# Performance work log

Measured on AMD Instinct MI355X. Metric: run time of the kernel, lower is better.

Reference implementation:

```python
import jax, jax.numpy as jnp
import numpy as np

EPS = 1e-5

def _conv3x3(x, w, b):
    # NCHW, OIHW, 3x3 stride 1 pad 1
    y = jax.lax.conv_general_dilated(x, w, window_strides=(1, 1),
                                     padding=((1, 1), (1, 1)),
                                     dimension_numbers=('NCHW', 'OIHW', 'NCHW'))
    return y + b[None, :, None, None]

def _pool_upsample(x, k):
    # adaptive avg pool to (H/k, W/k) then nearest block-upsample back
    B, C, H, W = x.shape
    p = x.reshape(B, C, H // k, k, W // k, k).mean(axis=(3, 5))
    return jnp.repeat(jnp.repeat(p, k, axis=2), k, axis=3)

def setup_inputs() -> dict:
    key = jax.random.key(0)
    ks = jax.random.split(key, 12)
    B, C, H, W = 32, 8, 300, 300
    d = {
        'x': jax.random.normal(ks[0], (B, C, H, W), jnp.float32),
        'w5': jax.random.normal(ks[1], (8, 16, 3, 3), jnp.float32) * 0.1,
        'b5': jnp.zeros((8,), jnp.float32),
        'w10': jax.random.normal(ks[2], (8, 16, 3, 3), jnp.float32) * 0.1,
        'b10': jnp.zeros((8,), jnp.float32),
        'w15': jax.random.normal(ks[3], (8, 16, 3, 3), jnp.float32) * 0.1,
        'b15': jnp.zeros((8,), jnp.float32),
        'gw': jax.random.normal(ks[4], (8, 24, 3, 3), jnp.float32) * 0.1,
        'gb': jnp.zeros((8,), jnp.float32),
        'mw': jax.random.normal(ks[5], (8, 24, 3, 3), jnp.float32) * 0.1,
        'mb': jnp.zeros((8,), jnp.float32),
        'gamma': jnp.ones((8,), jnp.float32),
        'beta': jnp.zeros((8,), jnp.float32),
    }
    return d

def reference(x, w5, b5, w10, b10, w15, b15, gw, gb, mw, mb, gamma, beta):
    up5 = _pool_upsample(x, 5)    # [B,8,300,300]
    up10 = _pool_upsample(x, 10)
    up15 = _pool_upsample(x, 15)
    c5 = _conv3x3(jnp.concatenate([x, up5], axis=1), w5, b5)
    c10 = _conv3x3(jnp.concatenate([x, up10], axis=1), w10, b10)
    c15 = _conv3x3(jnp.concatenate([x, up15], axis=1), w15, b15)
    g_in = jnp.concatenate([c5, c10, c15], axis=1)  # [B,24,H,W]
    # gated conv, activation=None: conv(g_in) * sigmoid(mask_conv(g_in))
    y = _conv3x3(g_in, gw, gb) * jax.nn.sigmoid(_conv3x3(g_in, mw, mb))
    # batch norm (training-mode batch stats, biased var, as torch default)
    mean = y.mean(axis=(0, 2, 3), keepdims=True)
    var = ((y - mean) ** 2).mean(axis=(0, 2, 3), keepdims=True)
    y = (y - mean) * jax.lax.rsqrt(var + EPS)
    return y * gamma[None, :, None, None] + beta[None, :, None, None]
```

## Files before the change

### kernel.cpp

```cpp
#include <hip/hip_runtime.h>
#include <math.h>

typedef __bf16 bfrag __attribute__((ext_vector_type(8)));
typedef __bf16 bf16x4 __attribute__((ext_vector_type(4)));
typedef __bf16 bf16x8 __attribute__((ext_vector_type(8)));
typedef float f32x4 __attribute__((ext_vector_type(4)));

#define BN 32
#define HH 300
#define WW 300
#define HW 90000
#define NPX (BN * HW)

#define GX 10
#define GY 19
#define CPX 612
#define XPX 720
#define CWSTRIDE 4896

#define P5I_BYTE_OFF   0
#define P10I_BYTE_OFF  1843200
#define P15I_BYTE_OFF  2304000
#define CWB_BYTE_OFF   2508800
#define GWB_BYTE_OFF   2524160
#define STAT_BYTE_OFF  2531328
#define SS_BYTE_OFF    2539520
#define XBF_BYTE_OFF   2539584
#define XBF_END        (XBF_BYTE_OFF + (size_t)NPX * 16)
#define GW3_BYTE_OFF   XBF_END
#define NEW3_END       (GW3_BYTE_OFF + 9216)

#define XU3_OFF   0
#define P5_OFF3   11520
#define P10_OFF3  12160
#define P15_OFF3  12400
#define CW0_OFF3  12592
#define CW1_OFF3  22384
#define LDS3_SIZE 32176

__device__ __forceinline__ short f2bf(float f) {
    union { float f; unsigned u; } v;
    v.f = f;
    unsigned r = v.u + 0x7FFF + ((v.u >> 16) & 1);
    return (short)(r >> 16);
}

__device__ __forceinline__ float bf2f(unsigned short s) {
    union { unsigned u; float f; } v;
    v.u = ((unsigned)s) << 16;
    return v.f;
}

__device__ __forceinline__ void setup_body(int gid, int gstride,
                                           const float* __restrict__ w5,
                                           const float* __restrict__ w10,
                                           const float* __restrict__ w15,
                                           const float* __restrict__ gw,
                                           const float* __restrict__ mw,
                                           short* __restrict__ cBg,
                                           short* __restrict__ gBg,
                                           short* __restrict__ gB3,
                                           double* __restrict__ stats) {
    for (int idx = gid; idx < 7680; idx += gstride) {
        int s = idx / 2560, rem = idx % 2560;
        int n = rem / 160, r2 = rem % 160;
        int tap = r2 / 16, ci = r2 % 16;
        float v = 0.f;
        if (n < 8 && tap < 9) {
            const float* W = (s == 0) ? w5 : ((s == 1) ? w10 : w15);
            v = W[(n * 16 + ci) * 9 + tap];
        }
        cBg[idx] = f2bf(v);
    }
    for (int idx = gid; idx < 3584; idx += gstride) {
        int n = idx / 224, r2 = idx % 224;
        int blk = r2 / 8, cj = r2 % 8;
        float v = 0.f;
        if (blk < 27) {
            int tap = blk / 3, ci24 = (blk % 3) * 8 + cj;
            if (n < 8) v = gw[(n * 24 + ci24) * 9 + tap];
            else       v = mw[((n - 8) * 24 + ci24) * 9 + tap];
        }
        gBg[idx] = f2bf(v);
    }
    if (gB3) {
        for (int idx = gid; idx < 4608; idx += gstride) {
            int s = idx / 1536, rem = idx % 1536;
            int n = rem / 96, r2 = rem % 96;
            int slot = r2 / 8, cj = r2 % 8;
            float v = 0.f;
            if (slot < 9) {
                int ci24 = s * 8 + cj;
                if (n < 8) v = gw[(n * 24 + ci24) * 9 + slot];
                else       v = mw[((n - 8) * 24 + ci24) * 9 + slot];
            }
            gB3[idx] = f2bf(v);
        }
    }
    for (int idx = gid; idx < 16 * 64; idx += gstride) stats[idx] = 0.0;
}

__global__ void k_setup(const float* __restrict__ w5, const float* __restrict__ w10,
                        const float* __restrict__ w15, const float* __restrict__ gw,
                        const float* __restrict__ mw, short* __restrict__ cBg,
                        short* __restrict__ gBg, double* __restrict__ stats) {
    setup_body(threadIdx.x, 256, w5, w10, w15, gw, mw, cBg, gBg, nullptr, stats);
}

__global__ __launch_bounds__(256) void k_xbf(const float* __restrict__ x,
                                             unsigned short* __restrict__ xbf,
                                             const float* __restrict__ w5,
                                             const float* __restrict__ w10,
                                             const float* __restrict__ w15,
                                             const float* __restrict__ gw,
                                             const float* __restrict__ mw,
                                             short* __restrict__ cBg,
                                             short* __restrict__ gBg,
                                             short* __restrict__ gB3,
                                             double* __restrict__ stats) {
    const int b = blockIdx.y;
    const int px = blockIdx.x * 256 + threadIdx.x;
    if (px < HW) {
        const float* xp = x + (size_t)b * 8 * HW + px;
        bf16x8 pk;
#pragma unroll
        for (int ch = 0; ch < 8; ch++) pk[ch] = (__bf16)xp[(size_t)ch * HW];
        *(bf16x8*)&xbf[((size_t)b * HW + px) * 8] = pk;
    }
    if (blockIdx.y == 0 && blockIdx.x < 16) {
        int gid = blockIdx.x * 256 + threadIdx.x;
        setup_body(gid, 4096, w5, w10, w15, gw, mw, cBg, gBg, gB3, stats);
    }
}

__global__ __launch_bounds__(256) void k_pool5b(const unsigned short* __restrict__ xbf,
                                                unsigned short* __restrict__ p5i) {
    int id = blockIdx.x * 256 + threadIdx.x;
    int b = id / 3600, cell = id % 3600;
    int pi = cell / 60, pj = cell % 60;
    const unsigned short* base = xbf + ((size_t)b * HW + pi * 5 * WW + pj * 5) * 8;
    float s[8] = {0.f, 0.f, 0.f, 0.f, 0.f, 0.f, 0.f, 0.f};
#pragma unroll
    for (int u = 0; u < 5; u++)
#pragma unroll
        for (int v = 0; v < 5; v++) {
            bf16x8 vv = *(const bf16x8*)&base[(u * WW + v) * 8];
#pragma unroll
            for (int ch = 0; ch < 8; ch++) s[ch] += (float)vv[ch];
        }
    bf16x8 pk;
#pragma unroll
    for (int ch = 0; ch < 8; ch++) pk[ch] = (__bf16)(s[ch] * 0.04f);
    *(bf16x8*)&p5i[((size_t)b * 3600 + cell) * 8] = pk;
}

__global__ void k_poolD(const unsigned short* __restrict__ p5i,
                        unsigned short* __restrict__ p10i,
                        unsigned short* __restrict__ p15i) {
    int id = blockIdx.x * 256 + threadIdx.x;
    if (id < 230400) {
        int bc = id / 900, cell = id % 900;
        int b = bc >> 3, c = bc & 7;
        int pi = cell / 30, pj = cell % 30;
        const unsigned short* base = p5i + ((size_t)b * 3600) * 8 + c;
        float s = bf2f(base[((2 * pi) * 60 + 2 * pj) * 8]) +
                  bf2f(base[((2 * pi) * 60 + 2 * pj + 1) * 8]) +
                  bf2f(base[((2 * pi + 1) * 60 + 2 * pj) * 8]) +
                  bf2f(base[((2 * pi + 1) * 60 + 2 * pj + 1) * 8]);
        p10i[((size_t)b * 900 + cell) * 8 + c] = (unsigned short)f2bf(s * 0.25f);
    } else if (id < 332800) {
        int id2 = id - 230400;
        int bc = id2 / 400, cell = id2 % 400;
        int b = bc >> 3, c = bc & 7;
        int pi = cell / 20, pj = cell % 20;
        const unsigned short* base = p5i + ((size_t)b * 3600) * 8 + c;
        float s = 0.f;
#pragma unroll
        for (int u = 0; u < 3; u++)
#pragma unroll
            for (int v = 0; v < 3; v++)
                s += bf2f(base[((3 * pi + u) * 60 + 3 * pj + v) * 8]);
        p15i[((size_t)b * 400 + cell) * 8 + c] = (unsigned short)f2bf(s * (1.f / 9.f));
    }
}

template <int K, int PCOLS>
__device__ __forceinline__ void c_phase3(char* LDSp, int cwOff, int patchOff,
                                         const unsigned short* __restrict__ cBs,
                                         const float* __restrict__ bias,
                                         int pr0, int pc0,
                                         int r0, int c0, int lane, int wid, bool edge) {
    constexpr int T0[5] = {0, 2, 4, 6, 8};
    constexpr int T1[5] = {1, 3, 5, 7, 8};
    const int n = lane & 15, quad = lane >> 4;
    const int qh = quad >> 1, ql = quad & 1;
    bfrag wfr[5];
#pragma unroll
    for (int km = 0; km < 5; km++) {
        int tapw = km * 2 + qh;
        wfr[km] = *(const bfrag*)&cBs[(n * 10 + tapw) * 16 + ql * 8];
    }
    const int srow = patchOff - pr0 * (PCOLS * 16);
    const int scol = -(pc0 << 4);
    float bO[4];
#pragma unroll
    for (int r = 0; r < 4; r++) bO[r] = bias[(quad & 1) * 4 + r];

    for (int g = wid; g < 39; g += 4) {
        int px = g * 16 + n;
        if (px > 611) px = 611;
        int rp = (int)((unsigned)px / 34u);
        int cp = px - rp * 34;
        int xb = (rp * 36 + cp) * 16;
        int rowB[3], colB[3];
#pragma unroll
        for (int d = 0; d < 3; d++) {
            rowB[d] = (int)(((unsigned)(r0 - 2 + rp + d + K) / (unsigned)K) * (PCOLS * 16)) + srow;
            colB[d] = (int)(((unsigned)(c0 - 2 + cp + d + K) / (unsigned)K) << 4) + scol;
        }
        f32x4 acc = {0.f, 0.f, 0.f, 0.f};
#pragma unroll
        for (int km = 0; km < 5; km++) {
            int au0 = rowB[T0[km] / 3] + colB[T0[km] % 3];
            int au1 = rowB[T1[km] / 3] + colB[T1[km] % 3];
            int ax0 = xb + ((T0[km] / 3) * 36 + (T0[km] % 3)) * 16;
            int ax1 = xb + ((T1[km] / 3) * 36 + (T1[km] % 3)) * 16;
            int au = qh ? au1 : au0;
            int ax = qh ? ax1 : ax0;
            int ad = ql ? au : ax;
            acc = __builtin_amdgcn_mfma_f32_16x16x32_bf16(
                wfr[km], *(const bfrag*)(LDSp + ad), acc, 0, 0, 0);
        }
        if (quad < 2) {
            bf16x4 pk;
#pragma unroll
            for (int r = 0; r < 4; r++) pk[r] = (__bf16)(acc[r] + bO[r]);
            if (edge) {
                int ra = r0 - 1 + rp, ca = c0 - 1 + cp;
                if (ra < 0 || ra >= HH || ca < 0 || ca >= WW) {
#pragma unroll
                    for (int r = 0; r < 4; r++) pk[r] = (__bf16)0.f;
                }
            }
            *(bf16x4*)(LDSp + cwOff + px * 16 + quad * 8) = pk;
        }
    }
}

__device__ __forceinline__ void gate_partial(const char* LDSp, int cwOff,
                                             const unsigned short* __restrict__ gB3s,
                                             int lane, int wid, f32x4* acc) {
    const int n = lane & 15, quad = lane >> 4;
    bfrag gfr[3];
    int goffB[3];
#pragma unroll
    for (int km = 0; km < 3; km++) {
        int slot = km * 4 + quad;
        int tap = (slot > 8) ? 8 : slot;
        gfr[km] = *(const bfrag*)&gB3s[(n * 12 + slot) * 8];
        int di = tap / 3, dj = tap - di * 3;
        goffB[km] = (di * 34 + dj) * 16;
    }
#pragma unroll
    for (int gi = 0; gi < 8; gi++) {
        int g = wid + 4 * gi;
        int px = g * 16 + n;
        int off0 = cwOff + ((px >> 5) * 34 + (px & 31)) * 16;
#pragma unroll
        for (int km = 0; km < 3; km++)
            acc[gi] = __builtin_amdgcn_mfma_f32_16x16x32_bf16(
                gfr[km], *(const bfrag*)(LDSp + off0 + goffB[km]), acc[gi], 0, 0, 0);
    }
}

__global__ __launch_bounds__(256, 5) void k_fused3(
    const unsigned short* __restrict__ xbf,
    const unsigned short* __restrict__ p5i, const unsigned short* __restrict__ p10i,
    const unsigned short* __restrict__ p15i,
    const unsigned short* __restrict__ cBg, const unsigned short* __restrict__ gB3,
    const float* __restrict__ b5, const float* __restrict__ b10, const float* __restrict__ b15,
    const float* __restrict__ gb, const float* __restrict__ mb,
    float* __restrict__ out, double* __restrict__ stats) {
    __shared__ __align__(16) char LDS[LDS3_SIZE];

    const int b = blockIdx.z;
    const int r0 = blockIdx.y * 16, c0 = blockIdx.x * 32;
    const int t = threadIdx.x, lane = t & 63, wid = t >> 6;
    const bool edge = (blockIdx.x == 0) | (blockIdx.x == GX - 1) |
                      (blockIdx.y == 0) | (blockIdx.y == GY - 1);

    const int pr0_5 = (r0 + 3) / 5, pc0_5 = (c0 + 3) / 5;
    const int pr0_10 = (r0 + 8) / 10, pc0_10 = (c0 + 8) / 10;
    const int pr0_15 = (r0 + 13) / 15, pc0_15 = (c0 + 13) / 15;

#pragma unroll
    for (int it = 0; it < 3; it++) {
        int idx = t + 256 * it;
        if (idx < XPX) {
            int i = idx / 36, j = idx - i * 36;
            int ra = r0 - 2 + i, ca = c0 - 2 + j;
            uint4 v = {0u, 0u, 0u, 0u};
            if (ra >= 0 && ra < HH && ca >= 0 && ca < WW)
                v = *(const uint4*)&xbf[((size_t)b * HW + ra * WW + ca) * 8];
            *(uint4*)(LDS + XU3_OFF + idx * 16) = v;
        }
    }
    if (t < 67) {
        const unsigned short* src;
        int off;
        bool valid;
        if (t < 40) {
            int a = t >> 3, cc = t & 7;
            int ci = pr0_5 - 1 + a, cj = pc0_5 - 1 + cc;
            valid = (ci >= 0) && (ci < 60) && (cj >= 0) && (cj < 60);
            src = p5i + ((size_t)b * 3600 + ci * 60 + cj) * 8;
            off = P5_OFF3 + t * 16;
        } else if (t < 55) {
            int i2 = t - 40;
            int a = i2 / 5, cc = i2 % 5;
            int ci = pr0_10 - 1 + a, cj = pc0_10 - 1 + cc;
            valid = (ci >= 0) && (ci < 30) && (cj >= 0) && (cj < 30);
            src = p10i + ((size_t)b * 900 + ci * 30 + cj) * 8;
            off = P10_OFF3 + i2 * 16;
        } else {
            int i2 = t - 55;
            int a = i2 >> 2, cc = i2 & 3;
            int ci = pr0_15 - 1 + a, cj = pc0_15 - 1 + cc;
            valid = (ci >= 0) && (ci < 20) && (cj >= 0) && (cj < 20);
            src = p15i + ((size_t)b * 400 + ci * 20 + cj) * 8;
            off = P15_OFF3 + i2 * 16;
        }
        uint4 v = {0u, 0u, 0u, 0u};
        if (valid) v = *(const uint4*)src;
        *(uint4*)(LDS + off) = v;
    }
    __syncthreads();

    f32x4 acc[8];
#pragma unroll
    for (int gi = 0; gi < 8; gi++) acc[gi] = (f32x4){0.f, 0.f, 0.f, 0.f};

    c_phase3<5, 8>(LDS, CW0_OFF3, P5_OFF3, cBg, b5, pr0_5, pc0_5, r0, c0, lane, wid, edge);
    __syncthreads();
    gate_partial(LDS, CW0_OFF3, gB3, lane, wid, acc);
    c_phase3<10, 5>(LDS, CW1_OFF3, P10_OFF3, cBg + 2560, b10, pr0_10, pc0_10, r0, c0, lane, wid, edge);
    __syncthreads();
    gate_partial(LDS, CW1_OFF3, gB3 + 1536, lane, wid, acc);
    c_phase3<15, 4>(LDS, CW0_OFF3, P15_OFF3, cBg + 5120, b15, pr0_15, pc0_15, r0, c0, lane, wid, edge);
    __syncthreads();
    gate_partial(LDS, CW0_OFF3, gB3 + 3072, lane, wid, acc);

    const int n = lane & 15, quad = lane >> 4;
    float gO[4], mO[4];
#pragma unroll
    for (int r = 0; r < 4; r++) {
        gO[r] = gb[(quad & 1) * 4 + r];
        mO[r] = mb[(quad & 1) * 4 + r];
    }
    float ls[4] = {0.f, 0.f, 0.f, 0.f}, ls2[4] = {0.f, 0.f, 0.f, 0.f};
#pragma unroll
    for (int gi = 0; gi < 8; gi++) {
        int g = wid + 4 * gi;
        int px = g * 16 + n;
        int rr = px >> 5, cc = px & 31;
        int ra = r0 + rr, ca = c0 + cc;
        bool wr = !edge || (ra < HH && ca < WW);
#pragma unroll
        for (int reg = 0; reg < 4; reg++) {
            float val;
            if (quad < 2) val = acc[gi][reg] + gO[reg];
            else          val = __builtin_amdgcn_rcpf(1.f + __expf(-(acc[gi][reg] + mO[reg])));
            float other = __shfl_xor(val, 32);
            if (quad < 2 && wr) {
                float y = val * other;
                int ch = quad * 4 + reg;
                out[(size_t)(b * 8 + ch) * HW + (size_t)ra * WW + ca] = y;
                ls[reg] += y;
                ls2[reg] += y * y;
            }
        }
    }
#pragma unroll
    for (int m = 1; m < 16; m <<= 1) {
#pragma unroll
        for (int r = 0; r < 4; r++) {
            ls[r] += __shfl_xor(ls[r], m);
            ls2[r] += __shfl_xor(ls2[r], m);
        }
    }
    if (n == 0 && quad < 2) {
        int hash = (blockIdx.x + GX * blockIdx.y + GX * GY * blockIdx.z) & 63;
#pragma unroll
        for (int r = 0; r < 4; r++) {
            atomicAdd(&stats[(quad * 4 + r) * 64 + hash], (double)ls[r]);
            atomicAdd(&stats[(8 + quad * 4 + r) * 64 + hash], (double)ls2[r]);
        }
    }
}

__global__ void k_pool5(const float* __restrict__ x, unsigned short* __restrict__ p5i) {
    int id = blockIdx.x * 256 + threadIdx.x;
    int bc = id / 3600, cell = id % 3600;
    int b = bc >> 3, c = bc & 7;
    int pi = cell / 60, pj = cell % 60;
    const float* rp = x + (size_t)bc * HW + pi * 5 * WW + pj * 5;
    float s = 0.f;
#pragma unroll
    for (int u = 0; u < 5; u++)
#pragma unroll
        for (int v = 0; v < 5; v++) s += rp[u * WW + v];
    p5i[((size_t)b * 3600 + cell) * 8 + c] = (unsigned short)f2bf(s * 0.04f);
}

template <int K, int PW>
__device__ __forceinline__ void up_load(const unsigned short* __restrict__ pooled,
                                        int b, int r0, int c0, int t, uint4* v) {
#pragma unroll
    for (int it = 0; it < 3; it++) {
        int idx = t + 256 * it;
        uint4 val = {0u, 0u, 0u, 0u};
        if (idx < XPX) {
            int i = idx / 36, j = idx - i * 36;
            int ra = r0 - 2 + i, ca = c0 - 2 + j;
            if (ra >= 0 && ra < HH && ca >= 0 && ca < WW) {
                int pi = (int)((unsigned)ra / K);
                int pj = (int)((unsigned)ca / K);
                val = *(const uint4*)&pooled[((size_t)b * (PW * PW) + pi * PW + pj) * 8];
            }
        }
        v[it] = val;
    }
}

__device__ __forceinline__ void up_store(short* xuU, int t, const uint4* v) {
#pragma unroll
    for (int it = 0; it < 3; it++) {
        int idx = t + 256 * it;
        if (idx < XPX) *(uint4*)&xuU[idx * 8] = v[it];
    }
}

__device__ __forceinline__ void c_phase(const short* xuX, const short* xuU,
                                        short* cwP,
                                        const unsigned short* __restrict__ cBs,
                                        const float* __restrict__ bias,
                                        int r0, int c0, int lane, int wid, bool edge) {
    const int n = lane & 15, quad = lane >> 4;
    const int qh = quad >> 1, ql = quad & 1;
    const short* xbase = ql ? xuU : xuX;
    bfrag wfr[5];
    int dpoff[5];
#pragma unroll
    for (int km = 0; km < 5; km++) {
        int tapw = km * 2 + qh;
        int tapa = (tapw > 8) ? 8 : tapw;
        wfr[km] = *(const bfrag*)&cBs[(n * 10 + tapw) * 16 + ql * 8];
        dpoff[km] = ((tapa / 3) * 36 + tapa % 3) * 8;
    }
    float bO[4];
#pragma unroll
    for (int r = 0; r < 4; r++) bO[r] = bias[(quad & 1) * 4 + r];

    for (int g = wid; g < 39; g += 4) {
        int px = g * 16 + n;
        if (px > 611) px = 611;
        int rp = (int)((unsigned)px / 34u);
        int cp = px - rp * 34;
        int pb = (rp * 36 + cp) * 8;
        f32x4 acc = {0.f, 0.f, 0.f, 0.f};
#pragma unroll
        for (int km = 0; km < 5; km++)
            acc = __builtin_amdgcn_mfma_f32_16x16x32_bf16(
                wfr[km], *(const bfrag*)&xbase[pb + dpoff[km]], acc, 0, 0, 0);
        if (quad < 2) {
            bf16x4 pk;
#pragma unroll
            for (int r = 0; r < 4; r++) pk[r] = (__bf16)(acc[r] + bO[r]);
            if (edge) {
                int ra = r0 - 1 + rp, ca = c0 - 1 + cp;
                if (ra < 0 || ra >= HH || ca < 0 || ca >= WW) {
#pragma unroll
                    for (int r = 0; r < 4; r++) pk[r] = (__bf16)0.f;
                }
            }
            *(bf16x4*)&cwP[px * 8 + quad * 4] = pk;
        }
    }
}

template <bool XBF>
__global__ __launch_bounds__(256, 3) void k_fused(
    const float* __restrict__ x, const unsigned short* __restrict__ xbf,
    const unsigned short* __restrict__ p5i, const unsigned short* __restrict__ p10i,
    const unsigned short* __restrict__ p15i,
    const unsigned short* __restrict__ cBg, const unsigned short* __restrict__ gBg,
    const float* __restrict__ b5, const float* __restrict__ b10, const float* __restrict__ b15,
    const float* __restrict__ gb, const float* __restrict__ mb,
    float* __restrict__ out, double* __restrict__ stats) {
    __shared__ __align__(16) short xuX[XPX * 8];
    __shared__ __align__(16) short xuU[XPX * 8];
    __shared__ __align__(16) short cwS[3 * CWSTRIDE];

    const int b = blockIdx.z;
    const int r0 = blockIdx.y * 16, c0 = blockIdx.x * 32;
    const int t = threadIdx.x, lane = t & 63, wid = t >> 6;
    const bool edge = (blockIdx.x == 0) | (blockIdx.x == GX - 1) |
                      (blockIdx.y == 0) | (blockIdx.y == GY - 1);

    uint4 upv[3];
    up_load<5, 60>(p5i, b, r0, c0, t, upv);

    if constexpr (XBF) {
#pragma unroll
        for (int it = 0; it < 3; it++) {
            int idx = t + 256 * it;
            if (idx < XPX) {
                int i = idx / 36, j = idx - i * 36;
                int ra = r0 - 2 + i, ca = c0 - 2 + j;
                uint4 v = {0u, 0u, 0u, 0u};
                if (ra >= 0 && ra < HH && ca >= 0 && ca < WW)
                    v = *(const uint4*)&xbf[((size_t)b * HW + ra * WW + ca) * 8];
                *(uint4*)&xuX[idx * 8] = v;
            }
        }
    } else {
        for (int idx = t; idx < 1440; idx += 256) {
            int cp = idx / 360, rem = idx % 360;
            int i = rem / 18, jp = rem % 18;
            int j = 2 * jp;
            int ra = r0 - 2 + i, ca = c0 - 2 + j;
            float2 v0 = {0.f, 0.f}, v1 = {0.f, 0.f};
            if (ra >= 0 && ra < HH && ca >= 0 && ca <= WW - 2) {
                size_t base = ((size_t)(b * 8 + 2 * cp) * HH + ra) * WW + ca;
                v0 = *(const float2*)&x[base];
                v1 = *(const float2*)&x[base + HW];
            }
            unsigned pA = (unsigned short)f2bf(v0.x) | ((unsigned)(unsigned short)f2bf(v1.x) << 16);
            unsigned pB = (unsigned short)f2bf(v0.y) | ((unsigned)(unsigned short)f2bf(v1.y) << 16);
            int px = i * 36 + j;
            *(unsigned*)&xuX[px * 8 + 2 * cp] = pA;
            *(unsigned*)&xuX[(px + 1) * 8 + 2 * cp] = pB;
        }
    }
    up_store(xuU, t, upv);
    __syncthreads();

    c_phase(xuX, xuU, cwS, cBg, b5, r0, c0, lane, wid, edge);
    up_load<10, 30>(p10i, b, r0, c0, t, upv);
    __syncthreads();
    up_store(xuU, t, upv);
    __syncthreads();

    c_phase(xuX, xuU, cwS + CWSTRIDE, cBg + 2560, b10, r0, c0, lane, wid, edge);
    up_load<15, 20>(p15i, b, r0, c0, t, upv);
    __syncthreads();
    up_store(xuU, t, upv);
    __syncthreads();

    c_phase(xuX, xuU, cwS + 2 * CWSTRIDE, cBg + 5120, b15, r0, c0, lane, wid, edge);
    __syncthreads();

    const int n = lane & 15, quad = lane >> 4;
    bfrag gfr[7];
    int goff[7];
#pragma unroll
    for (int km = 0; km < 7; km++) {
        int blkw = km * 4 + quad;
        int blka = (blkw > 26) ? 26 : blkw;
        gfr[km] = *(const bfrag*)&gBg[(n * 28 + blkw) * 8];
        int tap = blka / 3, cig = blka - tap * 3;
        goff[km] = cig * CWSTRIDE + ((tap / 3) * 34 + tap % 3) * 8;
    }
    float gO[4], mO[4];
#pragma unroll
    for (int r = 0; r < 4; r++) {
        gO[r] = gb[(quad & 1) * 4 + r];
        mO[r] = mb[(quad & 1) * 4 + r];
    }
    float ls[4] = {0.f, 0.f, 0.f, 0.f}, ls2[4] = {0.f, 0.f, 0.f, 0.f};

    for (int g = wid; g < 32; g += 4) {
        int px = g * 16 + n;
        int rr = px >> 5, cc = px & 31;
        int off0 = (rr * 34 + cc) * 8;
        f32x4 acc = {0.f, 0.f, 0.f, 0.f};
#pragma unroll
        for (int km = 0; km < 7; km++)
            acc = __builtin_amdgcn_mfma_f32_16x16x32_bf16(
                gfr[km], *(const bfrag*)&cwS[off0 + goff[km]], acc, 0, 0, 0);
        int ra = r0 + rr, ca = c0 + cc;
        bool wr = !edge || (ra < HH && ca < WW);
#pragma unroll
        for (int reg = 0; reg < 4; reg++) {
            float val;
            if (quad < 2) val = acc[reg] + gO[reg];
            else          val = __builtin_amdgcn_rcpf(1.f + __expf(-(acc[reg] + mO[reg])));
            float other = __shfl_xor(val, 32);
            if (quad < 2 && wr) {
                float y = val * other;
                int ch = quad * 4 + reg;
                out[(size_t)(b * 8 + ch) * HW + (size_t)ra * WW + ca] = y;
                ls[reg] += y;
                ls2[reg] += y * y;
            }
        }
    }
#pragma unroll
    for (int m = 1; m < 16; m <<= 1) {
#pragma unroll
        for (int r = 0; r < 4; r++) {
            ls[r] += __shfl_xor(ls[r], m);
            ls2[r] += __shfl_xor(ls2[r], m);
        }
    }
    if (n == 0 && quad < 2) {
        int hash = (blockIdx.x + GX * blockIdx.y + GX * GY * blockIdx.z) & 63;
#pragma unroll
        for (int r = 0; r < 4; r++) {
            atomicAdd(&stats[(quad * 4 + r) * 64 + hash], (double)ls[r]);
            atomicAdd(&stats[(8 + quad * 4 + r) * 64 + hash], (double)ls2[r]);
        }
    }
}

__global__ void k_stats(const double* __restrict__ stats, const float* __restrict__ gamma,
                        const float* __restrict__ beta, float* __restrict__ ss) {
    __shared__ double red[16][16];
    int t = threadIdx.x;
    int row = t >> 4, col = t & 15;
    double s = stats[row * 64 + col] + stats[row * 64 + col + 16] +
               stats[row * 64 + col + 32] + stats[row * 64 + col + 48];
    red[row][col] = s;
    __syncthreads();
    if (t < 16) {
        double tot = 0.0;
#pragma unroll
        for (int i = 0; i < 16; i++) tot += red[t][i];
        red[t][0] = tot;
    }
    __syncthreads();
    if (t < 8) {
        double N = (double)NPX;
        double mean = red[t][0] / N;
        double var = red[8 + t][0] / N - mean * mean;
        double scale = (double)gamma[t] / sqrt(var + 1e-5);
        ss[t] = (float)scale;
        ss[8 + t] = (float)((double)beta[t] - mean * scale);
    }
}

__global__ void k_norm(float* __restrict__ out, const float* __restrict__ ss) {
    int i = blockIdx.x * 256 + threadIdx.x;
    if (i < (BN * 8 * HW) / 4) {
        int plane = (i * 4) / HW;
        int ch = plane & 7;
        float sc = ss[ch], sh = ss[8 + ch];
        float4* p = (float4*)out + i;
        float4 v = *p;
        v.x = v.x * sc + sh;
        v.y = v.y * sc + sh;
        v.z = v.z * sc + sh;
        v.w = v.w * sc + sh;
        *p = v;
    }
}

extern "C" void kernel_launch(void* const* d_in, const int* in_sizes, int n_in,
                              void* d_out, int out_size, void* d_ws, size_t ws_size,
                              hipStream_t stream) {
    const float* x = (const float*)d_in[0];
    const float* w5 = (const float*)d_in[1];
    const float* b5 = (const float*)d_in[2];
    const float* w10 = (const float*)d_in[3];
    const float* b10 = (const float*)d_in[4];
    const float* w15 = (const float*)d_in[5];
    const float* b15 = (const float*)d_in[6];
    const float* gw = (const float*)d_in[7];
    const float* gb = (const float*)d_in[8];
    const float* mw = (const float*)d_in[9];
    const float* mb = (const float*)d_in[10];
    const float* gamma = (const float*)d_in[11];
    const float* beta = (const float*)d_in[12];
    float* out = (float*)d_out;

    unsigned short* p5i = (unsigned short*)((char*)d_ws + P5I_BYTE_OFF);
    unsigned short* p10i = (unsigned short*)((char*)d_ws + P10I_BYTE_OFF);
    unsigned short* p15i = (unsigned short*)((char*)d_ws + P15I_BYTE_OFF);
    short* cBg = (short*)((char*)d_ws + CWB_BYTE_OFF);
    short* gBg = (short*)((char*)d_ws + GWB_BYTE_OFF);
    double* stats = (double*)((char*)d_ws + STAT_BYTE_OFF);
    float* ss = (float*)((char*)d_ws + SS_BYTE_OFF);
    unsigned short* xbf = (unsigned short*)((char*)d_ws + XBF_BYTE_OFF);
    short* gB3 = (short*)((char*)d_ws + GW3_BYTE_OFF);

    dim3 grid(GX, GY, BN);
    if (ws_size >= NEW3_END) {
        k_xbf<<<dim3(352, 32), 256, 0, stream>>>(x, xbf, w5, w10, w15, gw, mw,
                                                 cBg, gBg, gB3, stats);
        k_pool5b<<<450, 256, 0, stream>>>(xbf, p5i);
        k_poolD<<<1300, 256, 0, stream>>>(p5i, p10i, p15i);
        k_fused3<<<grid, 256, 0, stream>>>(xbf, p5i, p10i, p15i,
                                           (const unsigned short*)cBg, (const unsigned short*)gB3,
                                           b5, b10, b15, gb, mb, out, stats);
    } else if (ws_size >= XBF_END) {
        k_xbf<<<dim3(352, 32), 256, 0, stream>>>(x, xbf, w5, w10, w15, gw, mw,
                                                 cBg, gBg, nullptr, stats);
        k_pool5b<<<450, 256, 0, stream>>>(xbf, p5i);
        k_poolD<<<1300, 256, 0, stream>>>(p5i, p10i, p15i);
        k_fused<true><<<grid, 256, 0, stream>>>(x, xbf, p5i, p10i, p15i,
                                                (const unsigned short*)cBg, (const unsigned short*)gBg,
                                                b5, b10, b15, gb, mb, out, stats);
    } else {
        k_setup<<<1, 256, 0, stream>>>(w5, w10, w15, gw, mw, cBg, gBg, stats);
        k_pool5<<<3600, 256, 0, stream>>>(x, p5i);
        k_poolD<<<1300, 256, 0, stream>>>(p5i, p10i, p15i);
        k_fused<false><<<grid, 256, 0, stream>>>(x, xbf, p5i, p10i, p15i,
                                                 (const unsigned short*)cBg, (const unsigned short*)gBg,
                                                 b5, b10, b15, gb, mb, out, stats);
    }
    k_stats<<<1, 256, 0, stream>>>(stats, gamma, beta, ss);
    k_norm<<<(BN * 8 * HW / 4 + 255) / 256, 256, 0, stream>>>(out, ss);
}
```

Before: 424.6 us.

## Fuse pooling levels into one kernel and keep all three branch outputs in LDS

Merges the 5x5 pooling and the derived 10x10/15x15 pooling into one tiled kernel that stages a 30x30 xbf tile in shared memory, removing one launch and the round trip of p5i. The fused conv kernel now computes all three branch convolutions into separate LDS buffers, then runs a single 7-step MFMA gated conv over 24 channels. This replaces the earlier interleaved per-branch gate partial accumulation. LDS use grows to about 42KB per block, which may reduce occupancy below the 3-block launch bound, and the extra setup path for gB3 is dropped.

```diff
diff --git a/kernel.cpp b/kernel.cpp
--- a/kernel.cpp
+++ b/kernel.cpp
@@ -27,16 +27,13 @@
 #define SS_BYTE_OFF    2539520
 #define XBF_BYTE_OFF   2539584
 #define XBF_END        (XBF_BYTE_OFF + (size_t)NPX * 16)
-#define GW3_BYTE_OFF   XBF_END
-#define NEW3_END       (GW3_BYTE_OFF + 9216)
-
-#define XU3_OFF   0
-#define P5_OFF3   11520
-#define P10_OFF3  12160
-#define P15_OFF3  12400
-#define CW0_OFF3  12592
-#define CW1_OFF3  22384
-#define LDS3_SIZE 32176
+
+#define XU4_OFF   0
+#define P5_OFF4   11520
+#define P10_OFF4  12160
+#define P15_OFF4  12400
+#define CW4_OFF   12592
+#define LDS4_SIZE 41968
 
 __device__ __forceinline__ short f2bf(float f) {
     union { float f; unsigned u; } v;
@@ -59,7 +56,6 @@
                                            const float* __restrict__ mw,
                                            short* __restrict__ cBg,
                                            short* __restrict__ gBg,
-                                           short* __restrict__ gB3,
                                            double* __restrict__ stats) {
     for (int idx = gid; idx < 7680; idx += gstride) {
         int s = idx / 2560, rem = idx % 2560;
@@ -83,20 +79,6 @@
         }
         gBg[idx] = f2bf(v);
     }
-    if (gB3) {
-        for (int idx = gid; idx < 4608; idx += gstride) {
-            int s = idx / 1536, rem = idx % 1536;
-            int n = rem / 96, r2 = rem % 96;
-            int slot = r2 / 8, cj = r2 % 8;
-            float v = 0.f;
-            if (slot < 9) {
-                int ci24 = s * 8 + cj;
-                if (n < 8) v = gw[(n * 24 + ci24) * 9 + slot];
-                else       v = mw[((n - 8) * 24 + ci24) * 9 + slot];
-            }
-            gB3[idx] = f2bf(v);
-        }
-    }
     for (int idx = gid; idx < 16 * 64; idx += gstride) stats[idx] = 0.0;
 }
 
@@ -104,7 +86,7 @@
                         const float* __restrict__ w15, const float* __restrict__ gw,
                         const float* __restrict__ mw, short* __restrict__ cBg,
                         short* __restrict__ gBg, double* __restrict__ stats) {
-    setup_body(threadIdx.x, 256, w5, w10, w15, gw, mw, cBg, gBg, nullptr, stats);
+    setup_body(threadIdx.x, 256, w5, w10, w15, gw, mw, cBg, gBg, stats);
 }
 
 __global__ __launch_bounds__(256) void k_xbf(const float* __restrict__ x,
@@ -116,7 +98,6 @@
                                              const float* __restrict__ mw,
                                              short* __restrict__ cBg,
                                              short* __restrict__ gBg,
-                                             short* __restrict__ gB3,
                                              double* __restrict__ stats) {
     const int b = blockIdx.y;
     const int px = blockIdx.x * 256 + threadIdx.x;
@@ -129,29 +110,279 @@
     }
     if (blockIdx.y == 0 && blockIdx.x < 16) {
         int gid = blockIdx.x * 256 + threadIdx.x;
-        setup_body(gid, 4096, w5, w10, w15, gw, mw, cBg, gBg, gB3, stats);
-    }
-}
-
-__global__ __launch_bounds__(256) void k_pool5b(const unsigned short* __restrict__ xbf,
-                                                unsigned short* __restrict__ p5i) {
+        setup_body(gid, 4096, w5, w10, w15, gw, mw, cBg, gBg, stats);
+    }
+}
+
+__global__ __launch_bounds__(256) void k_poolAll(const unsigned short* __restrict__ xbf,
+                                                 unsigned short* __restrict__ p5i,
+                                                 unsigned short* __restrict__ p10i,
+                                                 unsigned short* __restrict__ p15i) {
+    __shared__ __align__(16) short xt[900 * 8];
+    __shared__ float p5t[36][8];
+    const int b = blockIdx.y;
+    const int bi = blockIdx.x / 10, bj = blockIdx.x % 10;
+    const int t = threadIdx.x;
+    for (int idx = t; idx < 900; idx += 256) {
+        int r = idx / 30, c = idx - r * 30;
+        *(uint4*)&xt[idx * 8] =
+            *(const uint4*)&xbf[((size_t)b * HW + (bi * 30 + r) * WW + bj * 30 + c) * 8];
+    }
+    __syncthreads();
+    if (t < 36) {
+        int pi = t / 6, pj = t - (t / 6) * 6;
+        float s[8] = {0.f, 0.f, 0.f, 0.f, 0.f, 0.f, 0.f, 0.f};
+#pragma unroll
+        for (int u = 0; u < 5; u++)
+#pragma unroll
+            for (int v = 0; v < 5; v++) {
+                bf16x8 vv = *(const bf16x8*)&xt[((pi * 5 + u) * 30 + pj * 5 + v) * 8];
+#pragma unroll
+                for (int ch = 0; ch < 8; ch++) s[ch] += (float)vv[ch];
+            }
+        bf16x8 pk;
+#pragma unroll
+        for (int ch = 0; ch < 8; ch++) {
+            float av = s[ch] * 0.04f;
+            p5t[t][ch] = av;
+            pk[ch] = (__bf16)av;
+        }
+        *(bf16x8*)&p5i[((size_t)b * 3600 + (bi * 6 + pi) * 60 + bj * 6 + pj) * 8] = pk;
+    }
+    __syncthreads();
+    if (t < 9) {
+        int pi = t / 3, pj = t - (t / 3) * 3;
+        bf16x8 pk;
+#pragma unroll
+        for (int ch = 0; ch < 8; ch++) {
+            float s = p5t[(2 * pi) * 6 + 2 * pj][ch] + p5t[(2 * pi) * 6 + 2 * pj + 1][ch] +
+                      p5t[(2 * pi + 1) * 6 + 2 * pj][ch] + p5t[(2 * pi + 1) * 6 + 2 * pj + 1][ch];
+            pk[ch] = (__bf16)(s * 0.25f);
+        }
+        *(bf16x8*)&p10i[((size_t)b * 900 + (bi * 3 + pi) * 30 + bj * 3 + pj) * 8] = pk;
+    } else if (t < 13) {
+        int i2 = t - 9;
+        int pi = i2 >> 1, pj = i2 & 1;
+        bf16x8 pk;
+#pragma unroll
+        for (int ch = 0; ch < 8; ch++) {
+            float s = 0.f;
+#pragma unroll
+            for (int u = 0; u < 3; u++)
+#pragma unroll
+                for (int v = 0; v < 3; v++) s += p5t[(3 * pi + u) * 6 + 3 * pj + v][ch];
+            pk[ch] = (__bf16)(s * (1.f / 9.f));
+        }
+        *(bf16x8*)&p15i[((size_t)b * 400 + (bi * 2 + pi) * 20 + bj * 2 + pj) * 8] = pk;
+    }
+}
+
+template <int K, int PCOLS>
+__device__ __forceinline__ void c_phase3(char* LDSp, int cwOff, int patchOff,
+                                         const unsigned short* __restrict__ cBs,
+                                         const float* __restrict__ bias,
+                                         int pr0, int pc0,
+                                         int r0, int c0, int lane, int wid, bool edge) {
+    constexpr int T0[5] = {0, 2, 4, 6, 8};
+    constexpr int T1[5] = {1, 3, 5, 7, 8};
+    const int n = lane & 15, quad = lane >> 4;
+    const int qh = quad >> 1, ql = quad & 1;
+    bfrag wfr[5];
+#pragma unroll
+    for (int km = 0; km < 5; km++) {
+        int tapw = km * 2 + qh;
+        wfr[km] = *(const bfrag*)&cBs[(n * 10 + tapw) * 16 + ql * 8];
+    }
+    const int srow = patchOff - pr0 * (PCOLS * 16);
+    const int scol = -(pc0 << 4);
+    float bO[4];
+#pragma unroll
+    for (int r = 0; r < 4; r++) bO[r] = bias[(quad & 1) * 4 + r];
+
+    for (int g = wid; g < 39; g += 4) {
+        int px = g * 16 + n;
+        if (px > 611) px = 611;
+        int rp = (int)((unsigned)px / 34u);
+        int cp = px - rp * 34;
+        int xb = (rp * 36 + cp) * 16;
+        int rowB[3], colB[3];
+#pragma unroll
+        for (int d = 0; d < 3; d++) {
+            rowB[d] = (int)(((unsigned)(r0 - 2 + rp + d + K) / (unsigned)K) * (PCOLS * 16)) + srow;
+            colB[d] = (int)(((unsigned)(c0 - 2 + cp + d + K) / (unsigned)K) << 4) + scol;
+        }
+        f32x4 acc = {0.f, 0.f, 0.f, 0.f};
+#pragma unroll
+        for (int km = 0; km < 5; km++) {
+            int au0 = rowB[T0[km] / 3] + colB[T0[km] % 3];
+            int au1 = rowB[T1[km] / 3] + colB[T1[km] % 3];
+            int ax0 = xb + ((T0[km] / 3) * 36 + (T0[km] % 3)) * 16;
+            int ax1 = xb + ((T1[km] / 3) * 36 + (T1[km] % 3)) * 16;
+            int au = qh ? au1 : au0;
+            int ax = qh ? ax1 : ax0;
+            int ad = ql ? au : ax;
+            acc = __builtin_amdgcn_mfma_f32_16x16x32_bf16(
+                wfr[km], *(const bfrag*)(LDSp + ad), acc, 0, 0, 0);
+        }
+        if (quad < 2) {
+            bf16x4 pk;
+#pragma unroll
+            for (int r = 0; r < 4; r++) pk[r] = (__bf16)(acc[r] + bO[r]);
+            if (edge) {
+                int ra = r0 - 1 + rp, ca = c0 - 1 + cp;
+                if (ra < 0 || ra >= HH || ca < 0 || ca >= WW) {
+#pragma unroll
+                    for (int r = 0; r < 4; r++) pk[r] = (__bf16)0.f;
+                }
+            }
+            *(bf16x4*)(LDSp + cwOff + px * 16 + quad * 8) = pk;
+        }
+    }
+}
+
+__global__ __launch_bounds__(256, 3) void k_fused4(
+    const unsigned short* __restrict__ xbf,
+    const unsigned short* __restrict__ p5i, const unsigned short* __restrict__ p10i,
+    const unsigned short* __restrict__ p15i,
+    const unsigned short* __restrict__ cBg, const unsigned short* __restrict__ gBg,
+    const float* __restrict__ b5, const float* __restrict__ b10, const float* __restrict__ b15,
+    const float* __restrict__ gb, const float* __restrict__ mb,
+    float* __restrict__ out, double* __restrict__ stats) {
+    __shared__ __align__(16) char LDS[LDS4_SIZE];
+
+    const int b = blockIdx.z;
+    const int r0 = blockIdx.y * 16, c0 = blockIdx.x * 32;
+    const int t = threadIdx.x, lane = t & 63, wid = t >> 6;
+    const bool edge = (blockIdx.x == 0) | (blockIdx.x == GX - 1) |
+                      (blockIdx.y == 0) | (blockIdx.y == GY - 1);
+
+    const int pr0_5 = (r0 + 3) / 5, pc0_5 = (c0 + 3) / 5;
+    const int pr0_10 = (r0 + 8) / 10, pc0_10 = (c0 + 8) / 10;
+    const int pr0_15 = (r0 + 13) / 15, pc0_15 = (c0 + 13) / 15;
+
+#pragma unroll
+    for (int it = 0; it < 3; it++) {
+        int idx = t + 256 * it;
+        if (idx < XPX) {
+            int i = idx / 36, j = idx - i * 36;
+            int ra = r0 - 2 + i, ca = c0 - 2 + j;
+            uint4 v = {0u, 0u, 0u, 0u};
+            if (ra >= 0 && ra < HH && ca >= 0 && ca < WW)
+                v = *(const uint4*)&xbf[((size_t)b * HW + ra * WW + ca) * 8];
+            *(uint4*)(LDS + XU4_OFF + idx * 16) = v;
+        }
+    }
+    if (t < 67) {
+        const unsigned short* src;
+        int off;
+        bool valid;
+        if (t < 40) {
+            int a = t >> 3, cc = t & 7;
+            int ci = pr0_5 - 1 + a, cj = pc0_5 - 1 + cc;
+            valid = (ci >= 0) && (ci < 60) && (cj >= 0) && (cj < 60);
+            src = p5i + ((size_t)b * 3600 + ci * 60 + cj) * 8;
+            off = P5_OFF4 + t * 16;
+        } else if (t < 55) {
+            int i2 = t - 40;
+            int a = i2 / 5, cc = i2 % 5;
+            int ci = pr0_10 - 1 + a, cj = pc0_10 - 1 + cc;
+            valid = (ci >= 0) && (ci < 30) && (cj >= 0) && (cj < 30);
+            src = p10i + ((size_t)b * 900 + ci * 30 + cj) * 8;
+            off = P10_OFF4 + i2 * 16;
+        } else {
+            int i2 = t - 55;
+            int a = i2 >> 2, cc = i2 & 3;
+            int ci = pr0_15 - 1 + a, cj = pc0_15 - 1 + cc;
+            valid = (ci >= 0) && (ci < 20) && (cj >= 0) && (cj < 20);
+            src = p15i + ((size_t)b * 400 + ci * 20 + cj) * 8;
+            off = P15_OFF4 + i2 * 16;
+        }
+        uint4 v = {0u, 0u, 0u, 0u};
+        if (valid) v = *(const uint4*)src;
+        *(uint4*)(LDS + off) = v;
+    }
+    __syncthreads();
+
+    c_phase3<5, 8>(LDS, CW4_OFF,          P5_OFF4,  cBg,        b5,  pr0_5,  pc0_5,  r0, c0, lane, wid, edge);
+    c_phase3<10, 5>(LDS, CW4_OFF + 9792,  P10_OFF4, cBg + 2560, b10, pr0_10, pc0_10, r0, c0, lane, wid, edge);
+    c_phase3<15, 4>(LDS, CW4_OFF + 19584, P15_OFF4, cBg + 5120, b15, pr0_15, pc0_15, r0, c0, lane, wid, edge);
+    __syncthreads();
+
+    const int n = lane & 15, quad = lane >> 4;
+    bfrag gfr[7];
+    int goff[7];
+#pragma unroll
+    for (int km = 0; km < 7; km++) {
+        int blkw = km * 4 + quad;
+        int blka = (blkw > 26) ? 26 : blkw;
+        gfr[km] = *(const bfrag*)&gBg[(n * 28 + blkw) * 8];
+        int tap = blka / 3, cig = blka - tap * 3;
+        goff[km] = cig * 9792 + ((tap / 3) * 34 + tap % 3) * 16;
+    }
+    float gO[4], mO[4];
+#pragma unroll
+    for (int r = 0; r < 4; r++) {
+        gO[r] = gb[(quad & 1) * 4 + r];
+        mO[r] = mb[(quad & 1) * 4 + r];
+    }
+    float ls[4] = {0.f, 0.f, 0.f, 0.f}, ls2[4] = {0.f, 0.f, 0.f, 0.f};
+
+    for (int g = wid; g < 32; g += 4) {
+        int px = g * 16 + n;
+        int rr = px >> 5, cc = px & 31;
+        int off0 = CW4_OFF + (rr * 34 + cc) * 16;
+        f32x4 acc = {0.f, 0.f, 0.f, 0.f};
+#pragma unroll
+        for (int km = 0; km < 7; km++)
+            acc = __builtin_amdgcn_mfma_f32_16x16x32_bf16(
+                gfr[km], *(const bfrag*)(LDS + off0 + goff[km]), acc, 0, 0, 0);
+        int ra = r0 + rr, ca = c0 + cc;
+        bool wr = !edge || (ra < HH && ca < WW);
+#pragma unroll
+        for (int reg = 0; reg < 4; reg++) {
+            float val;
+            if (quad < 2) val = acc[reg] + gO[reg];
+            else          val = __builtin_amdgcn_rcpf(1.f + __expf(-(acc[reg] + mO[reg])));
+            float other = __shfl_xor(val, 32);
+            if (quad < 2 && wr) {
+                float y = val * other;
+                int ch = quad * 4 + reg;
+                out[(size_t)(b * 8 + ch) * HW + (size_t)ra * WW + ca] = y;
+                ls[reg] += y;
+                ls2[reg] += y * y;
+            }
+        }
+    }
+#pragma unroll
+    for (int m = 1; m < 16; m <<= 1) {
+#pragma unroll
+        for (int r = 0; r < 4; r++) {
+            ls[r] += __shfl_xor(ls[r], m);
+            ls2[r] += __shfl_xor(ls2[r], m);
+        }
+    }
+    if (n == 0 && quad < 2) {
+        int hash = (blockIdx.x + GX * blockIdx.y + GX * GY * blockIdx.z) & 63;
+#pragma unroll
+        for (int r = 0; r < 4; r++) {
+            atomicAdd(&stats[(quad * 4 + r) * 64 + hash], (double)ls[r]);
+            atomicAdd(&stats[(8 + quad * 4 + r) * 64 + hash], (double)ls2[r]);
+        }
+    }
+}
+
+__global__ void k_pool5(const float* __restrict__ x, unsigned short* __restrict__ p5i) {
     int id = blockIdx.x * 256 + threadIdx.x;
-    int b = id / 3600, cell = id % 3600;
+    int bc = id / 3600, cell = id % 3600;
+    int b = bc >> 3, c = bc & 7;
     int pi = cell / 60, pj = cell % 60;
-    const unsigned short* base = xbf + ((size_t)b * HW + pi * 5 * WW + pj * 5) * 8;
-    float s[8] = {0.f, 0.f, 0.f, 0.f, 0.f, 0.f, 0.f, 0.f};
+    const float* rp = x + (size_t)bc * HW + pi * 5 * WW + pj * 5;
+    float s = 0.f;
 #pragma unroll
     for (int u = 0; u < 5; u++)
 #pragma unroll
-        for (int v = 0; v < 5; v++) {
-            bf16x8 vv = *(const bf16x8*)&base[(u * WW + v) * 8];
-#pragma unroll
-            for (int ch = 0; ch < 8; ch++) s[ch] += (float)vv[ch];
-        }
-    bf16x8 pk;
-#pragma unroll
-    for (int ch = 0; ch < 8; ch++) pk[ch] = (__bf16)(s[ch] * 0.04f);
-    *(bf16x8*)&p5i[((size_t)b * 3600 + cell) * 8] = pk;
+        for (int v = 0; v < 5; v++) s += rp[u * WW + v];
+    p5i[((size_t)b * 3600 + cell) * 8 + c] = (unsigned short)f2bf(s * 0.04f);
 }
 
 __global__ void k_poolD(const unsigned short* __restrict__ p5i,
@@ -184,234 +415,6 @@
     }
 }
 
-template <int K, int PCOLS>
-__device__ __forceinline__ void c_phase3(char* LDSp, int cwOff, int patchOff,
-                                         const unsigned short* __restrict__ cBs,
-                                         const float* __restrict__ bias,
-                                         int pr0, int pc0,
-                                         int r0, int c0, int lane, int wid, bool edge) {
-    constexpr int T0[5] = {0, 2, 4, 6, 8};
-    constexpr int T1[5] = {1, 3, 5, 7, 8};
-    const int n = lane & 15, quad = lane >> 4;
-    const int qh = quad >> 1, ql = quad & 1;
-    bfrag wfr[5];
-#pragma unroll
-    for (int km = 0; km < 5; km++) {
-        int tapw = km * 2 + qh;
-        wfr[km] = *(const bfrag*)&cBs[(n * 10 + tapw) * 16 + ql * 8];
-    }
-    const int srow = patchOff - pr0 * (PCOLS * 16);
-    const int scol = -(pc0 << 4);
-    float bO[4];
-#pragma unroll
-    for (int r = 0; r < 4; r++) bO[r] = bias[(quad & 1) * 4 + r];
-
-    for (int g = wid; g < 39; g += 4) {
-        int px = g * 16 + n;
-        if (px > 611) px = 611;
-        int rp = (int)((unsigned)px / 34u);
-        int cp = px - rp * 34;
-        int xb = (rp * 36 + cp) * 16;
-        int rowB[3], colB[3];
-#pragma unroll
-        for (int d = 0; d < 3; d++) {
-            rowB[d] = (int)(((unsigned)(r0 - 2 + rp + d + K) / (unsigned)K) * (PCOLS * 16)) + srow;
-            colB[d] = (int)(((unsigned)(c0 - 2 + cp + d + K) / (unsigned)K) << 4) + scol;
-        }
-        f32x4 acc = {0.f, 0.f, 0.f, 0.f};
-#pragma unroll
-        for (int km = 0; km < 5; km++) {
-            int au0 = rowB[T0[km] / 3] + colB[T0[km] % 3];
-            int au1 = rowB[T1[km] / 3] + colB[T1[km] % 3];
-            int ax0 = xb + ((T0[km] / 3) * 36 + (T0[km] % 3)) * 16;
-            int ax1 = xb + ((T1[km] / 3) * 36 + (T1[km] % 3)) * 16;
-            int au = qh ? au1 : au0;
-            int ax = qh ? ax1 : ax0;
-            int ad = ql ? au : ax;
-            acc = __builtin_amdgcn_mfma_f32_16x16x32_bf16(
-                wfr[km], *(const bfrag*)(LDSp + ad), acc, 0, 0, 0);
-        }
-        if (quad < 2) {
-            bf16x4 pk;
-#pragma unroll
-            for (int r = 0; r < 4; r++) pk[r] = (__bf16)(acc[r] + bO[r]);
-            if (edge) {
-                int ra = r0 - 1 + rp, ca = c0 - 1 + cp;
-                if (ra < 0 || ra >= HH || ca < 0 || ca >= WW) {
-#pragma unroll
-                    for (int r = 0; r < 4; r++) pk[r] = (__bf16)0.f;
-                }
-            }
-            *(bf16x4*)(LDSp + cwOff + px * 16 + quad * 8) = pk;
-        }
-    }
-}
-
-__device__ __forceinline__ void gate_partial(const char* LDSp, int cwOff,
-                                             const unsigned short* __restrict__ gB3s,
-                                             int lane, int wid, f32x4* acc) {
-    const int n = lane & 15, quad = lane >> 4;
-    bfrag gfr[3];
-    int goffB[3];
-#pragma unroll
-    for (int km = 0; km < 3; km++) {
-        int slot = km * 4 + quad;
-        int tap = (slot > 8) ? 8 : slot;
-        gfr[km] = *(const bfrag*)&gB3s[(n * 12 + slot) * 8];
-        int di = tap / 3, dj = tap - di * 3;
-        goffB[km] = (di * 34 + dj) * 16;
-    }
-#pragma unroll
-    for (int gi = 0; gi < 8; gi++) {
-        int g = wid + 4 * gi;
-        int px = g * 16 + n;
-        int off0 = cwOff + ((px >> 5) * 34 + (px & 31)) * 16;
-#pragma unroll
-        for (int km = 0; km < 3; km++)
-            acc[gi] = __builtin_amdgcn_mfma_f32_16x16x32_bf16(
-                gfr[km], *(const bfrag*)(LDSp + off0 + goffB[km]), acc[gi], 0, 0, 0);
-    }
-}
-
-__global__ __launch_bounds__(256, 5) void k_fused3(
-    const unsigned short* __restrict__ xbf,
-    const unsigned short* __restrict__ p5i, const unsigned short* __restrict__ p10i,
-    const unsigned short* __restrict__ p15i,
-    const unsigned short* __restrict__ cBg, const unsigned short* __restrict__ gB3,
-    const float* __restrict__ b5, const float* __restrict__ b10, const float* __restrict__ b15,
-    const float* __restrict__ gb, const float* __restrict__ mb,
-    float* __restrict__ out, double* __restrict__ stats) {
-    __shared__ __align__(16) char LDS[LDS3_SIZE];
-
-    const int b = blockIdx.z;
-    const int r0 = blockIdx.y * 16, c0 = blockIdx.x * 32;
-    const int t = threadIdx.x, lane = t & 63, wid = t >> 6;
-    const bool edge = (blockIdx.x == 0) | (blockIdx.x == GX - 1) |
-                      (blockIdx.y == 0) | (blockIdx.y == GY - 1);
-
-    const int pr0_5 = (r0 + 3) / 5, pc0_5 = (c0 + 3) / 5;
-    const int pr0_10 = (r0 + 8) / 10, pc0_10 = (c0 + 8) / 10;
-    const int pr0_15 = (r0 + 13) / 15, pc0_15 = (c0 + 13) / 15;
-
-#pragma unroll
-    for (int it = 0; it < 3; it++) {
-        int idx = t + 256 * it;
-        if (idx < XPX) {
-            int i = idx / 36, j = idx - i * 36;
-            int ra = r0 - 2 + i, ca = c0 - 2 + j;
-            uint4 v = {0u, 0u, 0u, 0u};
-            if (ra >= 0 && ra < HH && ca >= 0 && ca < WW)
-                v = *(const uint4*)&xbf[((size_t)b * HW + ra * WW + ca) * 8];
-            *(uint4*)(LDS + XU3_OFF + idx * 16) = v;
-        }
-    }
-    if (t < 67) {
-        const unsigned short* src;
-        int off;
-        bool valid;
-        if (t < 40) {
-            int a = t >> 3, cc = t & 7;
-            int ci = pr0_5 - 1 + a, cj = pc0_5 - 1 + cc;
-            valid = (ci >= 0) && (ci < 60) && (cj >= 0) && (cj < 60);
-            src = p5i + ((size_t)b * 3600 + ci * 60 + cj) * 8;
-            off = P5_OFF3 + t * 16;
-        } else if (t < 55) {
-            int i2 = t - 40;
-            int a = i2 / 5, cc = i2 % 5;
-            int ci = pr0_10 - 1 + a, cj = pc0_10 - 1 + cc;
-            valid = (ci >= 0) && (ci < 30) && (cj >= 0) && (cj < 30);
-            src = p10i + ((size_t)b * 900 + ci * 30 + cj) * 8;
-            off = P10_OFF3 + i2 * 16;
-        } else {
-            int i2 = t - 55;
-            int a = i2 >> 2, cc = i2 & 3;
-            int ci = pr0_15 - 1 + a, cj = pc0_15 - 1 + cc;
-            valid = (ci >= 0) && (ci < 20) && (cj >= 0) && (cj < 20);
-            src = p15i + ((size_t)b * 400 + ci * 20 + cj) * 8;
-            off = P15_OFF3 + i2 * 16;
-        }
-        uint4 v = {0u, 0u, 0u, 0u};
-        if (valid) v = *(const uint4*)src;
-        *(uint4*)(LDS + off) = v;
-    }
-    __syncthreads();
-
-    f32x4 acc[8];
-#pragma unroll
-    for (int gi = 0; gi < 8; gi++) acc[gi] = (f32x4){0.f, 0.f, 0.f, 0.f};
-
-    c_phase3<5, 8>(LDS, CW0_OFF3, P5_OFF3, cBg, b5, pr0_5, pc0_5, r0, c0, lane, wid, edge);
-    __syncthreads();
-    gate_partial(LDS, CW0_OFF3, gB3, lane, wid, acc);
-    c_phase3<10, 5>(LDS, CW1_OFF3, P10_OFF3, cBg + 2560, b10, pr0_10, pc0_10, r0, c0, lane, wid, edge);
-    __syncthreads();
-    gate_partial(LDS, CW1_OFF3, gB3 + 1536, lane, wid, acc);
-    c_phase3<15, 4>(LDS, CW0_OFF3, P15_OFF3, cBg + 5120, b15, pr0_15, pc0_15, r0, c0, lane, wid, edge);
-    __syncthreads();
-    gate_partial(LDS, CW0_OFF3, gB3 + 3072, lane, wid, acc);
-
-    const int n = lane & 15, quad = lane >> 4;
-    float gO[4], mO[4];
-#pragma unroll
-    for (int r = 0; r < 4; r++) {
-        gO[r] = gb[(quad & 1) * 4 + r];
-        mO[r] = mb[(quad & 1) * 4 + r];
-    }
-    float ls[4] = {0.f, 0.f, 0.f, 0.f}, ls2[4] = {0.f, 0.f, 0.f, 0.f};
-#pragma unroll
-    for (int gi = 0; gi < 8; gi++) {
-        int g = wid + 4 * gi;
-        int px = g * 16 + n;
-        int rr = px >> 5, cc = px & 31;
-        int ra = r0 + rr, ca = c0 + cc;
-        bool wr = !edge || (ra < HH && ca < WW);
-#pragma unroll
-        for (int reg = 0; reg < 4; reg++) {
-            float val;
-            if (quad < 2) val = acc[gi][reg] + gO[reg];
-            else          val = __builtin_amdgcn_rcpf(1.f + __expf(-(acc[gi][reg] + mO[reg])));
-            float other = __shfl_xor(val, 32);
-            if (quad < 2 && wr) {
-                float y = val * other;
-                int ch = quad * 4 + reg;
-                out[(size_t)(b * 8 + ch) * HW + (size_t)ra * WW + ca] = y;
-                ls[reg] += y;
-                ls2[reg] += y * y;
-            }
-        }
-    }
-#pragma unroll
-    for (int m = 1; m < 16; m <<= 1) {
-#pragma unroll
-        for (int r = 0; r < 4; r++) {
-            ls[r] += __shfl_xor(ls[r], m);
-            ls2[r] += __shfl_xor(ls2[r], m);
-        }
-    }
-    if (n == 0 && quad < 2) {
-        int hash = (blockIdx.x + GX * blockIdx.y + GX * GY * blockIdx.z) & 63;
-#pragma unroll
-        for (int r = 0; r < 4; r++) {
-            atomicAdd(&stats[(quad * 4 + r) * 64 + hash], (double)ls[r]);
-            atomicAdd(&stats[(8 + quad * 4 + r) * 64 + hash], (double)ls2[r]);
-        }
-    }
-}
-
-__global__ void k_pool5(const float* __restrict__ x, unsigned short* __restrict__ p5i) {
-    int id = blockIdx.x * 256 + threadIdx.x;
-    int bc = id / 3600, cell = id % 3600;
-    int b = bc >> 3, c = bc & 7;
-    int pi = cell / 60, pj = cell % 60;
-    const float* rp = x + (size_t)bc * HW + pi * 5 * WW + pj * 5;
-    float s = 0.f;
-#pragma unroll
-    for (int u = 0; u < 5; u++)
-#pragma unroll
-        for (int v = 0; v < 5; v++) s += rp[u * WW + v];
-    p5i[((size_t)b * 3600 + cell) * 8 + c] = (unsigned short)f2bf(s * 0.04f);
-}
-
 template <int K, int PW>
 __device__ __forceinline__ void up_load(const unsigned short* __restrict__ pooled,
                                         int b, int r0, int c0, int t, uint4* v) {
@@ -488,9 +491,8 @@
     }
 }
 
-template <bool XBF>
-__global__ __launch_bounds__(256, 3) void k_fused(
-    const float* __restrict__ x, const unsigned short* __restrict__ xbf,
+__global__ __launch_bounds__(256, 3) void k_fused_fb(
+    const float* __restrict__ x,
     const unsigned short* __restrict__ p5i, const unsigned short* __restrict__ p10i,
     const unsigned short* __restrict__ p15i,
     const unsigned short* __restrict__ cBg, const unsigned short* __restrict__ gBg,
@@ -510,37 +512,22 @@
     uint4 upv[3];
     up_load<5, 60>(p5i, b, r0, c0, t, upv);
 
-    if constexpr (XBF) {
-#pragma unroll
-        for (int it = 0; it < 3; it++) {
-            int idx = t + 256 * it;
-            if (idx < XPX) {
-                int i = idx / 36, j = idx - i * 36;
-                int ra = r0 - 2 + i, ca = c0 - 2 + j;
-                uint4 v = {0u, 0u, 0u, 0u};
-                if (ra >= 0 && ra < HH && ca >= 0 && ca < WW)
-                    v = *(const uint4*)&xbf[((size_t)b * HW + ra * WW + ca) * 8];
-                *(uint4*)&xuX[idx * 8] = v;
-            }
-        }
-    } else {
-        for (int idx = t; idx < 1440; idx += 256) {
-            int cp = idx / 360, rem = idx % 360;
-            int i = rem / 18, jp = rem % 18;
-            int j = 2 * jp;
-            int ra = r0 - 2 + i, ca = c0 - 2 + j;
-            float2 v0 = {0.f, 0.f}, v1 = {0.f, 0.f};
-            if (ra >= 0 && ra < HH && ca >= 0 && ca <= WW - 2) {
-                size_t base = ((size_t)(b * 8 + 2 * cp) * HH + ra) * WW + ca;
-                v0 = *(const float2*)&x[base];
-                v1 = *(const float2*)&x[base + HW];
-            }
-            unsigned pA = (unsigned short)f2bf(v0.x) | ((unsigned)(unsigned short)f2bf(v1.x) << 16);
-            unsigned pB = (unsigned short)f2bf(v0.y) | ((unsigned)(unsigned short)f2bf(v1.y) << 16);
-            int px = i * 36 + j;
-            *(unsigned*)&xuX[px * 8 + 2 * cp] = pA;
-            *(unsigned*)&xuX[(px + 1) * 8 + 2 * cp] = pB;
-        }
+    for (int idx = t; idx < 1440; idx += 256) {
+        int cp = idx / 360, rem = idx % 360;
+        int i = rem / 18, jp = rem % 18;
+        int j = 2 * jp;
+        int ra = r0 - 2 + i, ca = c0 - 2 + j;
+        float2 v0 = {0.f, 0.f}, v1 = {0.f, 0.f};
+        if (ra >= 0 && ra < HH && ca >= 0 && ca <= WW - 2) {
+            size_t base = ((size_t)(b * 8 + 2 * cp) * HH + ra) * WW + ca;
+            v0 = *(const float2*)&x[base];
+            v1 = *(const float2*)&x[base + HW];
+        }
+        unsigned pA = (unsigned short)f2bf(v0.x) | ((unsigned)(unsigned short)f2bf(v1.x) << 16);
+        unsigned pB = (unsigned short)f2bf(v0.y) | ((unsigned)(unsigned short)f2bf(v1.y) << 16);
+        int px = i * 36 + j;
+        *(unsigned*)&xuX[px * 8 + 2 * cp] = pA;
+        *(unsigned*)&xuX[(px + 1) * 8 + 2 * cp] = pB;
     }
     up_store(xuU, t, upv);
     __syncthreads();
@@ -691,32 +678,22 @@
     double* stats = (double*)((char*)d_ws + STAT_BYTE_OFF);
     float* ss = (float*)((char*)d_ws + SS_BYTE_OFF);
     unsigned short* xbf = (unsigned short*)((char*)d_ws + XBF_BYTE_OFF);
-    short* gB3 = (short*)((char*)d_ws + GW3_BYTE_OFF);
 
     dim3 grid(GX, GY, BN);
-    if (ws_size >= NEW3_END) {
+    if (ws_size >= XBF_END) {
         k_xbf<<<dim3(352, 32), 256, 0, stream>>>(x, xbf, w5, w10, w15, gw, mw,
-                                                 cBg, gBg, gB3, stats);
-        k_pool5b<<<450, 256, 0, stream>>>(xbf, p5i);
-        k_poolD<<<1300, 256, 0, stream>>>(p5i, p10i, p15i);
-        k_fused3<<<grid, 256, 0, stream>>>(xbf, p5i, p10i, p15i,
-                                           (const unsigned short*)cBg, (const unsigned short*)gB3,
+                                                 cBg, gBg, stats);
+        k_poolAll<<<dim3(100, 32), 256, 0, stream>>>(xbf, p5i, p10i, p15i);
+        k_fused4<<<grid, 256, 0, stream>>>(xbf, p5i, p10i, p15i,
+                                           (const unsigned short*)cBg, (const unsigned short*)gBg,
                                            b5, b10, b15, gb, mb, out, stats);
-    } else if (ws_size >= XBF_END) {
-        k_xbf<<<dim3(352, 32), 256, 0, stream>>>(x, xbf, w5, w10, w15, gw, mw,
-                                                 cBg, gBg, nullptr, stats);
-        k_pool5b<<<450, 256, 0, stream>>>(xbf, p5i);
-        k_poolD<<<1300, 256, 0, stream>>>(p5i, p10i, p15i);
-        k_fused<true><<<grid, 256, 0, stream>>>(x, xbf, p5i, p10i, p15i,
-                                                (const unsigned short*)cBg, (const unsigned short*)gBg,
-                                                b5, b10, b15, gb, mb, out, stats);
     } else {
         k_setup<<<1, 256, 0, stream>>>(w5, w10, w15, gw, mw, cBg, gBg, stats);
         k_pool5<<<3600, 256, 0, stream>>>(x, p5i);
         k_poolD<<<1300, 256, 0, stream>>>(p5i, p10i, p15i);
-        k_fused<false><<<grid, 256, 0, stream>>>(x, xbf, p5i, p10i, p15i,
-                                                 (const unsigned short*)cBg, (const unsigned short*)gBg,
-                                                 b5, b10, b15, gb, mb, out, stats);
+        k_fused_fb<<<grid, 256, 0, stream>>>(x, p5i, p10i, p15i,
+                                             (const unsigned short*)cBg, (const unsigned short*)gBg,
+                                             b5, b10, b15, gb, mb, out, stats);
     }
     k_stats<<<1, 256, 0, stream>>>(stats, gamma, beta, ss);
     k_norm<<<(BN * 8 * HW / 4 + 255) / 256, 256, 0, stream>>>(out, ss);
```

New measurement: 383.6 us. 1.11x faster.
